# Kernel optimization log

Measured on AMD Instinct MI355X. Metric: run time of the kernel, lower is better.

Reference implementation:

```python
import jax, jax.numpy as jnp
import numpy as np

B = 16; DEMO = 5; COND = 50; QOI = 50
L = DEMO * (COND + 2 * QOI)  # 750
D = 1024; H = 16; HD = D // H; NL = 6; DFF = 4096
IN_DIM = 5; OUT_DIM = 2; MAXPOS = max(COND, QOI)
NEG = -1e9


def _build_consts():
    # token types per demo segment: 0=cond, 1=qoi_kv, 2=qoi_k (query)
    types, demo, pos = [], [], []
    for d in range(DEMO):
        types += [0] * COND + [1] * QOI + [2] * QOI
        demo += [d] * (COND + 2 * QOI)
        pos += list(range(COND)) + list(range(QOI)) + list(range(QOI))
    t = np.array(types); g = np.array(demo); p = np.array(pos)
    ti, tj = t[:, None], t[None, :]
    gi, gj = g[:, None], g[None, :]
    eye = np.arange(L)[:, None] == np.arange(L)[None, :]
    prev = (gj < gi) & (tj < 2)                      # attend to cond/qoi_kv of earlier demos
    same = (gj == gi) & ((tj == 0) | ((ti == 1) & (tj == 1)) | ((ti == 2) & eye))
    mask = prev | same                               # True = allowed
    out_idx = np.where(t == 2)[0]                    # qoi_k positions -> outputs
    return mask, p, out_idx


def setup_inputs():
    key = jax.random.key(0)
    ks = jax.random.split(key, 10)
    mask, pos, out_idx = _build_consts()
    s = 0.02
    return {
        'sequence': jax.random.normal(ks[0], (B, L, IN_DIM), jnp.float32),
        'pre_W': jax.random.normal(ks[1], (IN_DIM, D), jnp.float32) * s,
        'pre_b': jnp.zeros((D,), jnp.float32),
        'pe_table': jax.random.normal(ks[2], (MAXPOS, D), jnp.float32) * s,
        'Wqkv': jax.random.normal(ks[3], (NL, D, 3 * D), jnp.float32) * s,
        'bqkv': jnp.zeros((NL, 3 * D), jnp.float32),
        'Wo': jax.random.normal(ks[4], (NL, D, D), jnp.float32) * s,
        'bo': jnp.zeros((NL, D), jnp.float32),
        'ln1_g': jnp.ones((NL, D), jnp.float32), 'ln1_b': jnp.zeros((NL, D), jnp.float32),
        'ln2_g': jnp.ones((NL, D), jnp.float32), 'ln2_b': jnp.zeros((NL, D), jnp.float32),
        'W1': jax.random.normal(ks[5], (NL, D, DFF), jnp.float32) * s,
        'b1': jnp.zeros((NL, DFF), jnp.float32),
        'W2': jax.random.normal(ks[6], (NL, DFF, D), jnp.float32) * s,
        'b2': jnp.zeros((NL, D), jnp.float32),
        'post_W': jax.random.normal(ks[7], (D, OUT_DIM), jnp.float32) * s,
        'post_b': jnp.zeros((OUT_DIM,), jnp.float32),
        'basic_mask': jnp.asarray(mask),
        'index_pos': jnp.asarray(pos, jnp.int32),
        'out_idx': jnp.asarray(out_idx, jnp.int32),
    }


def _ln(x, g, b):
    m = jnp.mean(x, axis=-1, keepdims=True)
    v = jnp.var(x, axis=-1, keepdims=True)
    return (x - m) * jax.lax.rsqrt(v + 1e-5) * g + b


def _encoder(x, bias, Wqkv, bqkv, Wo, bo, ln1_g, ln1_b, ln2_g, ln2_b, W1, b1, W2, b2):
    scale = 1.0 / np.sqrt(HD)
    for l in range(NL):
        qkv = x @ Wqkv[l] + bqkv[l]                          # [B,L,3D]
        q, k, v = jnp.split(qkv, 3, axis=-1)
        hd = lambda t: t.reshape(B, L, H, HD).transpose(0, 2, 1, 3)
        q, k, v = hd(q), hd(k), hd(v)
        sc = jnp.einsum('bhqd,bhkd->bhqk', q, k) * scale + bias
        a = jax.nn.softmax(sc, axis=-1)
        o = jnp.einsum('bhqk,bhkd->bhqd', a, v).transpose(0, 2, 1, 3).reshape(B, L, D)
        x = _ln(x + o @ Wo[l] + bo[l], ln1_g[l], ln1_b[l])   # post-LN (torch default)
        h = jax.nn.gelu(x @ W1[l] + b1[l], approximate=False)
        x = _ln(x + h @ W2[l] + b2[l], ln2_g[l], ln2_b[l])
    return x


def reference(sequence, pre_W, pre_b, pe_table, Wqkv, bqkv, Wo, bo,
              ln1_g, ln1_b, ln2_g, ln2_b, W1, b1, W2, b2,
              post_W, post_b, basic_mask, index_pos, out_idx):
    x = sequence @ pre_W + pre_b + pe_table[index_pos]       # pre-projection + learned PE
    bias = jnp.where(basic_mask, 0.0, NEG)[None, None, :, :]  # ~basic_mask -> -inf additive
    x = _encoder(x, bias, Wqkv, bqkv, Wo, bo, ln1_g, ln1_b, ln2_g, ln2_b, W1, b1, W2, b2)
    y = x @ post_W + post_b                                  # [B,L,OUT_DIM]
    y = y[:, out_idx, :]                                     # select qoi_k outputs
    return y.reshape(B, DEMO, QOI, OUT_DIM)
```

## Files before the change

kernel.cpp:

```cpp
#include <hip/hip_runtime.h>


#define Bz  16
#define Lz  750
#define Dz  1024
#define Hz  16
#define HDz 64
#define NLz 6
#define DFFz 4096
#define Mz  (Bz*Lz)
#define MTt 94
#define VSTRIDE 768
#define QKVPART ((size_t)Bz*Hz*Lz*HDz)

typedef unsigned short u16;
typedef unsigned int   u32;
typedef unsigned long long u64;
typedef __attribute__((ext_vector_type(8))) short bf8;
typedef __attribute__((ext_vector_type(8))) unsigned short u16x8;
typedef __attribute__((ext_vector_type(4))) float f4;
typedef __attribute__((ext_vector_type(4))) unsigned short u16x4;

__device__ __forceinline__ u16 f2b(float f){
  u32 u = __builtin_bit_cast(u32, f);
  u += 0x7fffu + ((u >> 16) & 1u);
  return (u16)(u >> 16);
}
__device__ __forceinline__ u32 cvtpk(float a, float b){
  u32 r;
  asm("v_cvt_pk_bf16_f32 %0, %1, %2" : "=v"(r) : "v"(a), "v"(b));
  return r;
}
__device__ __forceinline__ void glds16(const void* g, void* l){
  __builtin_amdgcn_global_load_lds((const __attribute__((address_space(1))) void*)g,
                                   (__attribute__((address_space(3))) void*)l, 16, 0, 0);
}

__global__ __launch_bounds__(256) void k_mask(u64* __restrict__ mb){
  const int idx = blockIdx.x*256 + threadIdx.x;
  if (idx >= Lz*12) return;
  const int q = idx / 12, kt = idx - q*12;
  const int gq = q/150, rq = q - gq*150;
  const int tq = rq < 50 ? 0 : (rq < 100 ? 1 : 2);
  u64 m = 0;
  for (int j = 0; j < 64; j++){
    const int k = kt*64 + j;
    if (k >= Lz) break;
    const int gk = k/150, rk = k - gk*150;
    const int tk = rk < 50 ? 0 : (rk < 100 ? 1 : 2);
    const bool prev = (gk < gq) && (tk < 2);
    const bool same = (gk == gq) && ((tk == 0) || (tq == 1 && tk == 1) || (tq == 2 && k == q));
    if (prev || same) m |= (1ull << j);
  }
  mb[idx] = m;
}

__global__ __launch_bounds__(256) void k_embed(const float* __restrict__ seq,
    const float* __restrict__ preW, const float* __restrict__ preb,
    const float* __restrict__ pe, float* __restrict__ x, u16* __restrict__ xb){
  const int m = blockIdx.x, t = threadIdx.x;
  const int l = m % Lz;
  const int r = l % 150;
  const int p = r < 50 ? r : (r < 100 ? r - 50 : r - 100);
  const float s0 = seq[m*5+0], s1 = seq[m*5+1], s2 = seq[m*5+2],
              s3 = seq[m*5+3], s4 = seq[m*5+4];
  const int d = t*4;
  f4 acc = *(const f4*)&preb[d];
  acc += *(const f4*)&pe[p*Dz + d];
  acc += s0 * *(const f4*)&preW[0*Dz + d];
  acc += s1 * *(const f4*)&preW[1*Dz + d];
  acc += s2 * *(const f4*)&preW[2*Dz + d];
  acc += s3 * *(const f4*)&preW[3*Dz + d];
  acc += s4 * *(const f4*)&preW[4*Dz + d];
  *(f4*)&x[(size_t)m*Dz + d] = acc;
  u16x4 hv = { f2b(acc.x), f2b(acc.y), f2b(acc.z), f2b(acc.w) };
  *(u16x4*)&xb[(size_t)m*Dz + d] = hv;
}

__global__ __launch_bounds__(256) void k_transpose(const float* __restrict__ W,
    u16* __restrict__ Wt, int K, int ldw){
  __shared__ float tile[64][69];
  const int t = threadIdx.x;
  const int n0 = blockIdx.x*64, k0 = blockIdx.y*64;
  const int tx = t & 15, ty = t >> 4;
  #pragma unroll
  for (int i = 0; i < 4; i++){
    const int k = ty + i*16;
    *(f4*)&tile[k][tx*4] = *(const f4*)&W[(size_t)(k0+k)*ldw + n0 + tx*4];
  }
  __syncthreads();
  const int nx = t >> 2, kq = t & 3;
  u16 buf[16];
  #pragma unroll
  for (int e = 0; e < 16; e++)
    buf[e] = f2b(tile[kq*16 + e][nx]);
  u16x8 lo = { buf[0], buf[1], buf[2], buf[3], buf[4], buf[5], buf[6], buf[7] };
  u16x8 hi = { buf[8], buf[9], buf[10], buf[11], buf[12], buf[13], buf[14], buf[15] };
  u16* dst = &Wt[(size_t)(n0 + nx)*K + k0 + kq*16];
  *(u16x8*)dst = lo;
  *(u16x8*)(dst + 8) = hi;
}

template<int EPI>
__global__ __launch_bounds__(256, 4) void k_gemm(
    const u16* __restrict__ A, const u16* __restrict__ Bt,
    int M, int N, int K, int lda, int ldc, int col0, int NTn,
    const float* __restrict__ bias,
    float* __restrict__ xres, u16* __restrict__ outb, u16* __restrict__ vtb){
  const int id = blockIdx.x;
  const int PN = NTn << 3;
  const int panel = id / PN, rem = id - panel*PN;
  const int mt = panel*8 + (rem & 7);
  if (mt >= MTt) return;
  const int m0 = mt*128, n0 = (rem >> 3)*128;
  __shared__ u16 As[128*64];
  __shared__ u16 Bs[128*64];
  const int t = threadIdx.x;
  const int w = t >> 6, lane = t & 63;
  const int wm = (w >> 1)*64, wn = (w & 1)*64;
  const int cl = lane & 15, g4 = lane >> 4;
  f4 acc[4][4] = {};
  const int srow = t >> 3, sg = t & 7;
  const int scol = (sg ^ (srow & 7)) * 8;
  const int lds_off = srow*64 + sg*8;
  for (int k0 = 0; k0 < K; k0 += 64){
    #pragma unroll
    for (int c = 0; c < 4; c++){
      int ra = m0 + c*32 + srow; ra = ra < M ? ra : M-1;
      glds16(A + (size_t)ra*lda + k0 + scol, &As[c*2048 + lds_off]);
      const int rb = n0 + c*32 + srow;
      glds16(Bt + (size_t)rb*K + k0 + scol, &Bs[c*2048 + lds_off]);
    }
    __syncthreads();
    #pragma unroll
    for (int kk = 0; kk < 2; kk++){
      const int ko = ((kk*4 + g4) ^ (cl & 7)) * 8;
      bf8 af[4], bfr[4];
      #pragma unroll
      for (int i = 0; i < 4; i++) af[i]  = *(const bf8*)&As[(wm + i*16 + cl)*64 + ko];
      #pragma unroll
      for (int j = 0; j < 4; j++) bfr[j] = *(const bf8*)&Bs[(wn + j*16 + cl)*64 + ko];
      #pragma unroll
      for (int i = 0; i < 4; i++)
        #pragma unroll
        for (int j = 0; j < 4; j++)
          acc[i][j] = __builtin_amdgcn_mfma_f32_16x16x32_bf16(af[i], bfr[j], acc[i][j], 0, 0, 0);
    }
    __syncthreads();
  }
  const int rl = g4*4;
  #pragma unroll
  for (int i = 0; i < 4; i++){
    #pragma unroll
    for (int j = 0; j < 4; j++){
      const int gn = n0 + wn + j*16 + cl;
      const float bsv = bias ? bias[gn] : 0.f;
      if constexpr (EPI == 0){
        const int part = gn >> 10;
        const int hh = (gn >> 6) & 15;
        const int dd = gn & 63;
        const int gm0 = m0 + wm + i*16 + rl;
        if (part == 2){
          if (gm0 + 3 < M){
            const int b = gm0 / Lz, lr0 = gm0 - b*Lz;
            const float v0 = acc[i][j][0] + bsv, v1 = acc[i][j][1] + bsv;
            const float v2 = acc[i][j][2] + bsv, v3 = acc[i][j][3] + bsv;
            if (lr0 <= Lz - 4){
              u32* dst = (u32*)&vtb[((size_t)(b*Hz + hh)*HDz + dd)*VSTRIDE + lr0];
              dst[0] = cvtpk(v0, v1);
              dst[1] = cvtpk(v2, v3);
            } else {
              #pragma unroll
              for (int r = 0; r < 4; r++){
                const int gm = gm0 + r;
                const int br = gm / Lz, lr = gm - br*Lz;
                vtb[((size_t)(br*Hz + hh)*HDz + dd)*VSTRIDE + lr] = f2b(acc[i][j][r] + bsv);
              }
            }
          }
        } else {
          #pragma unroll
          for (int r = 0; r < 4; r++){
            const int gm = gm0 + r;
            if (gm < M){
              const int b = gm / Lz, lr = gm - b*Lz;
              outb[(size_t)part*QKVPART + ((size_t)(b*Hz + hh)*Lz + lr)*HDz + dd]
                  = f2b(acc[i][j][r] + bsv);
            }
          }
        }
      } else {
        #pragma unroll
        for (int r = 0; r < 4; r++){
          const int gm = m0 + wm + i*16 + rl + r;
          if (gm < M){
            const float v = acc[i][j][r] + bsv;
            if constexpr (EPI == 1){
              xres[(size_t)gm*ldc + col0 + gn] += v;
            } else {
              const float ge = 0.5f*v*(1.0f + erff(v*0.70710678f));
              outb[(size_t)gm*ldc + col0 + gn] = f2b(ge);
            }
          }
        }
      }
    }
  }
}

__global__ __launch_bounds__(64, 4) void k_attn(const u16* __restrict__ qb,
    const u16* __restrict__ kb, const u16* __restrict__ vt,
    const u64* __restrict__ mb, u16* __restrict__ ob){
  __shared__ u32 Ps[1024];
  const int t = threadIdx.x;
  const int cl = t & 15, g4 = t >> 4;
  const int id = blockIdx.x;
  const int xcd = id & 7, j = id >> 3;
  const int bh = xcd*32 + (j/12);
  const int bx = j - (j/12)*12;
  const int b = bh >> 4, h = bh & 15;
  const u16* qhp = qb + (size_t)bh*(Lz*HDz);
  const u16* khp = kb + (size_t)bh*(Lz*HDz);
  const u16* vhp = vt + (size_t)bh*(HDz*VSTRIDE);
  const float SC = 0.18033688011112042f;
  const f4 z4 = {0.f, 0.f, 0.f, 0.f};

  for (int half = 0; half < 2; half++){
    const int c = half ? (23 - bx) : bx;
    const int q0 = c*32;
    bf8 qfr[2][2];
    int qc[2];
    #pragma unroll
    for (int qf = 0; qf < 2; qf++){
      const int q = q0 + qf*16 + cl;
      qc[qf] = q < Lz ? q : Lz-1;
      #pragma unroll
      for (int kk = 0; kk < 2; kk++)
        qfr[qf][kk] = *(const bf8*)&qhp[(size_t)qc[qf]*HDz + kk*32 + g4*8];
    }
    int qmax = q0 + 31; if (qmax > Lz-1) qmax = Lz-1;
    const int gqm = qmax/150;
    int kmax = gqm*150 + 100; if (qmax + 1 > kmax) kmax = qmax + 1;
    const int nt = (kmax + 63) >> 6;

    f4 oacc[4][2] = {};
    float mrun[2] = {-1e30f, -1e30f}, lrun[2] = {0.f, 0.f};

    for (int kt = 0; kt < nt; kt++){
      const int kstart = kt*64;
      u32 mlo[2], mhi[2];
      #pragma unroll
      for (int qf = 0; qf < 2; qf++){
        const u64 m = mb[qc[qf]*12 + kt];
        mlo[qf] = (u32)m; mhi[qf] = (u32)(m >> 32);
      }
      f4 sacc[4][2];
      __builtin_amdgcn_s_setprio(1);
      #pragma unroll
      for (int kk = 0; kk < 2; kk++){
        bf8 kfr[4];
        #pragma unroll
        for (int kf = 0; kf < 4; kf++)
          kfr[kf] = *(const bf8*)&khp[(size_t)(kstart + kf*16 + cl)*HDz + kk*32 + g4*8];
        #pragma unroll
        for (int kf = 0; kf < 4; kf++)
          #pragma unroll
          for (int qf = 0; qf < 2; qf++)
            sacc[kf][qf] = __builtin_amdgcn_mfma_f32_16x16x32_bf16(kfr[kf], qfr[qf][kk],
                             kk == 0 ? z4 : sacc[kf][qf], 0, 0, 0);
      }
      __builtin_amdgcn_s_setprio(0);
      float own0 = -1e30f, own1 = -1e30f;
      #pragma unroll
      for (int kf = 0; kf < 4; kf++){
        #pragma unroll
        for (int rr = 0; rr < 4; rr++){
          const float s0 = sacc[kf][0][rr]*SC;
          const float s1 = sacc[kf][1][rr]*SC;
          sacc[kf][0][rr] = s0; sacc[kf][1][rr] = s1;
          own0 = fmaxf(own0, s0); own1 = fmaxf(own1, s1);
        }
      }
      own0 = fmaxf(own0, __shfl_xor(own0, 16)); own0 = fmaxf(own0, __shfl_xor(own0, 32));
      own1 = fmaxf(own1, __shfl_xor(own1, 16)); own1 = fmaxf(own1, __shfl_xor(own1, 32));
      const float mn0 = fmaxf(mrun[0], own0), mn1 = fmaxf(mrun[1], own1);
      const float sc0 = exp2f(mrun[0] - mn0), sc1 = exp2f(mrun[1] - mn1);
      float sum0 = 0.f, sum1 = 0.f;
      #pragma unroll
      for (int kf = 0; kf < 4; kf++){
        #pragma unroll
        for (int qf = 0; qf < 2; qf++){
          const float mn = qf ? mn1 : mn0;
          const u32 w16 = ((kf & 2) ? mhi[qf] : mlo[qf]) >> ((kf & 1)*16);
          const u32 wq = w16 >> (g4*4);
          f4 p;
          #pragma unroll
          for (int rr = 0; rr < 4; rr++){
            const float pe = exp2f(sacc[kf][qf][rr] - mn);
            p[rr] = ((wq >> rr) & 1u) ? pe : 0.f;
            if (qf == 0) sum0 += p[rr]; else sum1 += p[rr];
          }
          const u32 lo = cvtpk(p[0], p[1]);
          const u32 hi = cvtpk(p[2], p[3]);
          const int kk = kf >> 1;
          const int tg4 = ((kf & 1) << 1) | (g4 >> 1);
          const int widx = (qf*2 + kk)*256 + tg4*64 + cl*4 + (g4 & 1)*2;
          *(u64*)&Ps[widx] = ((u64)hi << 32) | lo;
        }
      }
      sum0 += __shfl_xor(sum0, 16); sum0 += __shfl_xor(sum0, 32);
      sum1 += __shfl_xor(sum1, 16); sum1 += __shfl_xor(sum1, 32);
      lrun[0] = lrun[0]*sc0 + sum0; mrun[0] = mn0;
      lrun[1] = lrun[1]*sc1 + sum1; mrun[1] = mn1;
      #pragma unroll
      for (int df = 0; df < 4; df++){
        oacc[df][0] *= sc0;
        oacc[df][1] *= sc1;
      }
      __builtin_amdgcn_s_setprio(1);
      #pragma unroll
      for (int kk = 0; kk < 2; kk++){
        bf8 vfr[4];
        #pragma unroll
        for (int df = 0; df < 4; df++)
          vfr[df] = *(const bf8*)&vhp[(size_t)(df*16 + cl)*VSTRIDE + kstart + kk*32 + g4*8];
        bf8 pw[2];
        #pragma unroll
        for (int qf = 0; qf < 2; qf++)
          pw[qf] = *(const bf8*)&Ps[(qf*2 + kk)*256 + g4*64 + cl*4];
        #pragma unroll
        for (int df = 0; df < 4; df++)
          #pragma unroll
          for (int qf = 0; qf < 2; qf++)
            oacc[df][qf] = __builtin_amdgcn_mfma_f32_16x16x32_bf16(vfr[df], pw[qf], oacc[df][qf], 0, 0, 0);
      }
      __builtin_amdgcn_s_setprio(0);
    }
    #pragma unroll
    for (int qf = 0; qf < 2; qf++){
      const int q = q0 + qf*16 + cl;
      if (q < Lz){
        const float inv = 1.f / lrun[qf];
        #pragma unroll
        for (int df = 0; df < 4; df++){
          u16x4 hv = { f2b(oacc[df][qf][0]*inv), f2b(oacc[df][qf][1]*inv),
                       f2b(oacc[df][qf][2]*inv), f2b(oacc[df][qf][3]*inv) };
          *(u16x4*)&ob[((size_t)b*Lz + q)*Dz + h*HDz + df*16 + g4*4] = hv;
        }
      }
    }
  }
}

__global__ __launch_bounds__(256) void k_ln(float* __restrict__ x, u16* __restrict__ xb,
    const float* __restrict__ g, const float* __restrict__ bb){
  const int m = blockIdx.x, t = threadIdx.x;
  float* xr = x + (size_t)m*Dz;
  f4 v = *(const f4*)&xr[t*4];
  float s = v.x + v.y + v.z + v.w;
  float q = v.x*v.x + v.y*v.y + v.z*v.z + v.w*v.w;
  #pragma unroll
  for (int off = 1; off < 64; off <<= 1){
    s += __shfl_xor(s, off);
    q += __shfl_xor(q, off);
  }
  __shared__ float ss[4], sq[4];
  const int w = t >> 6;
  if ((t & 63) == 0){ ss[w] = s; sq[w] = q; }
  __syncthreads();
  s = ss[0] + ss[1] + ss[2] + ss[3];
  q = sq[0] + sq[1] + sq[2] + sq[3];
  const float mean = s * (1.f/1024.f);
  const float var  = q * (1.f/1024.f) - mean*mean;
  const float rs = rsqrtf(var + 1e-5f);
  const f4 gg = *(const f4*)&g[t*4];
  const f4 bv = *(const f4*)&bb[t*4];
  f4 o;
  o.x = (v.x - mean)*rs*gg.x + bv.x;
  o.y = (v.y - mean)*rs*gg.y + bv.y;
  o.z = (v.z - mean)*rs*gg.z + bv.z;
  o.w = (v.w - mean)*rs*gg.w + bv.w;
  *(f4*)&xr[t*4] = o;
  u16x4 hv = { f2b(o.x), f2b(o.y), f2b(o.z), f2b(o.w) };
  *(u16x4*)&xb[(size_t)m*Dz + t*4] = hv;
}

__global__ __launch_bounds__(64) void k_out(const float* __restrict__ x,
    const float* __restrict__ pw, const float* __restrict__ pb, float* __restrict__ out){
  const int bid = blockIdx.x, lane = threadIdx.x;
  const int b = bid / 250, oi = bid - b*250;
  const int dd = oi / 50, qq = oi - dd*50;
  const int l = dd*150 + 100 + qq;
  const float* xr = x + ((size_t)b*Lz + l)*Dz;
  float a0 = 0.f, a1 = 0.f;
  #pragma unroll
  for (int c = 0; c < 4; c++){
    const int d = c*256 + lane*4;
    const f4 v  = *(const f4*)&xr[d];
    const f4 p0 = *(const f4*)&pw[2*d];
    const f4 p1 = *(const f4*)&pw[2*d + 4];
    a0 += v.x*p0.x + v.y*p0.z + v.z*p1.x + v.w*p1.z;
    a1 += v.x*p0.y + v.y*p0.w + v.z*p1.y + v.w*p1.w;
  }
  #pragma unroll
  for (int off = 32; off > 0; off >>= 1){
    a0 += __shfl_xor(a0, off);
    a1 += __shfl_xor(a1, off);
  }
  if (lane == 0){
    out[(size_t)bid*2 + 0] = a0 + pb[0];
    out[(size_t)bid*2 + 1] = a1 + pb[1];
  }
}

extern "C" void kernel_launch(void* const* d_in, const int* in_sizes, int n_in,
                              void* d_out, int out_size, void* d_ws, size_t ws_size,
                              hipStream_t stream){
  (void)in_sizes; (void)n_in; (void)out_size; (void)ws_size;
  const float* seq   = (const float*)d_in[0];
  const float* preW  = (const float*)d_in[1];
  const float* preb  = (const float*)d_in[2];
  const float* pe    = (const float*)d_in[3];
  const float* Wqkv  = (const float*)d_in[4];
  const float* bqkv  = (const float*)d_in[5];
  const float* Wo    = (const float*)d_in[6];
  const float* bo    = (const float*)d_in[7];
  const float* ln1g  = (const float*)d_in[8];
  const float* ln1b  = (const float*)d_in[9];
  const float* ln2g  = (const float*)d_in[10];
  const float* ln2b  = (const float*)d_in[11];
  const float* W1    = (const float*)d_in[12];
  const float* b1    = (const float*)d_in[13];
  const float* W2    = (const float*)d_in[14];
  const float* b2    = (const float*)d_in[15];
  const float* postW = (const float*)d_in[16];
  const float* postb = (const float*)d_in[17];
  float* out = (float*)d_out;

  char* ws = (char*)d_ws;
  float* x  = (float*)(ws + 0);
  u16*   xb = (u16*)(ws + 49152000);
  u16*   R  = (u16*)(ws + 73728000);
  u16* qB = R;
  u16* kB = R + QKVPART;
  u16* oB = R + 2*QKVPART;
  u16* vT = (u16*)(ws + 147456000);
  u16* wt = (u16*)(ws + 172621824);
  u64* mbp = (u64*)(ws + 178913280);
  u16* hB = R;

  k_mask<<<36, 256, 0, stream>>>(mbp);
  k_embed<<<Mz, 256, 0, stream>>>(seq, preW, preb, pe, x, xb);
  for (int l = 0; l < NLz; l++){
    k_transpose<<<dim3(48, 16), 256, 0, stream>>>(Wqkv + (size_t)l*1024*3072, wt, 1024, 3072);
    k_gemm<0><<<12*8*24, 256, 0, stream>>>(xb, wt, Mz, 3072, 1024, 1024, 0, 0, 24,
                                           bqkv + l*3072, nullptr, qB, vT);
    k_attn<<<3072, 64, 0, stream>>>(qB, kB, vT, mbp, oB);
    k_transpose<<<dim3(16, 16), 256, 0, stream>>>(Wo + (size_t)l*1024*1024, wt, 1024, 1024);
    k_gemm<1><<<12*8*8, 256, 0, stream>>>(oB, wt, Mz, 1024, 1024, 1024, 1024, 0, 8,
                                          bo + l*1024, x, nullptr, nullptr);
    k_ln<<<Mz, 256, 0, stream>>>(x, xb, ln1g + l*1024, ln1b + l*1024);
    for (int off = 0; off < 4096; off += 2048){
      k_transpose<<<dim3(32, 16), 256, 0, stream>>>(W1 + (size_t)l*1024*4096 + off, wt, 1024, 4096);
      k_gemm<2><<<12*8*16, 256, 0, stream>>>(xb, wt, Mz, 2048, 1024, 1024, 4096, off, 16,
                                             b1 + l*4096 + off, nullptr, hB, nullptr);
    }
    for (int koff = 0; koff < 4096; koff += 2048){
      k_transpose<<<dim3(16, 32), 256, 0, stream>>>(W2 + (size_t)l*4096*1024 + (size_t)koff*1024,
                                                    wt, 2048, 1024);
      k_gemm<1><<<12*8*8, 256, 0, stream>>>(hB + koff, wt, Mz, 1024, 2048, 4096, 1024, 0, 8,
                                            koff == 0 ? (b2 + l*1024) : nullptr, x, nullptr, nullptr);
    }
    k_ln<<<Mz, 256, 0, stream>>>(x, xb, ln2g + l*1024, ln2b + l*1024);
  }
  k_out<<<4000, 64, 0, stream>>>(x, postW, postb, out);
}
```

Before: 3.913 ms.

## Double-buffer GEMM LDS tiles with async prefetch two stages ahead

```diff
diff --git a/kernel.cpp b/kernel.cpp
--- a/kernel.cpp
+++ b/kernel.cpp
@@ -102,7 +102,7 @@
 }
 
 template<int EPI>
-__global__ __launch_bounds__(256, 4) void k_gemm(
+__global__ __launch_bounds__(256, 2) void k_gemm(
     const u16* __restrict__ A, const u16* __restrict__ Bt,
     int M, int N, int K, int lda, int ldc, int col0, int NTn,
     const float* __restrict__ bias,
@@ -113,8 +113,8 @@
   const int mt = panel*8 + (rem & 7);
   if (mt >= MTt) return;
   const int m0 = mt*128, n0 = (rem >> 3)*128;
-  __shared__ u16 As[128*64];
-  __shared__ u16 Bs[128*64];
+  __shared__ u16 As[2][128*64];
+  __shared__ u16 Bs[2][128*64];
   const int t = threadIdx.x;
   const int w = t >> 6, lane = t & 63;
   const int wm = (w >> 1)*64, wn = (w & 1)*64;
@@ -123,31 +123,49 @@
   const int srow = t >> 3, sg = t & 7;
   const int scol = (sg ^ (srow & 7)) * 8;
   const int lds_off = srow*64 + sg*8;
-  for (int k0 = 0; k0 < K; k0 += 64){
-    #pragma unroll
-    for (int c = 0; c < 4; c++){
-      int ra = m0 + c*32 + srow; ra = ra < M ? ra : M-1;
-      glds16(A + (size_t)ra*lda + k0 + scol, &As[c*2048 + lds_off]);
-      const int rb = n0 + c*32 + srow;
-      glds16(Bt + (size_t)rb*K + k0 + scol, &Bs[c*2048 + lds_off]);
-    }
-    __syncthreads();
+
+#define STG(c, kt) do {                                                          \
+    _Pragma("unroll")                                                            \
+    for (int cc = 0; cc < 4; cc++){                                              \
+      int ra = m0 + cc*32 + srow; ra = ra < M ? ra : M-1;                        \
+      glds16(A + (size_t)ra*lda + (size_t)(kt)*64 + scol, &As[c][cc*2048 + lds_off]); \
+      const int rb = n0 + cc*32 + srow;                                          \
+      glds16(Bt + (size_t)rb*K + (size_t)(kt)*64 + scol, &Bs[c][cc*2048 + lds_off]); \
+    }                                                                            \
+  } while(0)
+
+  const int nt = K >> 6;
+  STG(0, 0); STG(1, 1);
+  for (int kt = 0; kt < nt; kt++){
+    const int c = kt & 1;
+    if (kt + 1 < nt) asm volatile("s_waitcnt vmcnt(8)" ::: "memory");
+    else             asm volatile("s_waitcnt vmcnt(0)" ::: "memory");
+    __builtin_amdgcn_s_barrier();
+    bf8 af[4][2], bfr[4][2];
     #pragma unroll
     for (int kk = 0; kk < 2; kk++){
       const int ko = ((kk*4 + g4) ^ (cl & 7)) * 8;
-      bf8 af[4], bfr[4];
-      #pragma unroll
-      for (int i = 0; i < 4; i++) af[i]  = *(const bf8*)&As[(wm + i*16 + cl)*64 + ko];
-      #pragma unroll
-      for (int j = 0; j < 4; j++) bfr[j] = *(const bf8*)&Bs[(wn + j*16 + cl)*64 + ko];
+      #pragma unroll
+      for (int i = 0; i < 4; i++) af[i][kk]  = *(const bf8*)&As[c][(wm + i*16 + cl)*64 + ko];
+      #pragma unroll
+      for (int j = 0; j < 4; j++) bfr[j][kk] = *(const bf8*)&Bs[c][(wn + j*16 + cl)*64 + ko];
+    }
+    asm volatile("s_waitcnt lgkmcnt(0)" ::: "memory");
+    __builtin_amdgcn_sched_barrier(0);
+    __builtin_amdgcn_s_barrier();
+    if (kt + 2 < nt) STG(c, kt + 2);
+    __builtin_amdgcn_s_setprio(1);
+    #pragma unroll
+    for (int kk = 0; kk < 2; kk++)
       #pragma unroll
       for (int i = 0; i < 4; i++)
         #pragma unroll
         for (int j = 0; j < 4; j++)
-          acc[i][j] = __builtin_amdgcn_mfma_f32_16x16x32_bf16(af[i], bfr[j], acc[i][j], 0, 0, 0);
-    }
-    __syncthreads();
-  }
+          acc[i][j] = __builtin_amdgcn_mfma_f32_16x16x32_bf16(af[i][kk], bfr[j][kk], acc[i][j], 0, 0, 0);
+    __builtin_amdgcn_s_setprio(0);
+  }
+#undef STG
+
   const int rl = g4*4;
   #pragma unroll
   for (int i = 0; i < 4; i++){
```

Measured after the change: 4.497 ms. 14.9% more time.

## Split attention key tiles across two waves with LDS softmax merge

Applied to the files above, without the earlier changes.

```diff
diff --git a/kernel.cpp b/kernel.cpp
--- a/kernel.cpp
+++ b/kernel.cpp
@@ -102,7 +102,7 @@
 }
 
 template<int EPI>
-__global__ __launch_bounds__(256, 4) void k_gemm(
+__global__ __launch_bounds__(256, 5) void k_gemm(
     const u16* __restrict__ A, const u16* __restrict__ Bt,
     int M, int N, int K, int lda, int ldc, int col0, int NTn,
     const float* __restrict__ bias,
@@ -208,12 +208,14 @@
   }
 }
 
-__global__ __launch_bounds__(64, 4) void k_attn(const u16* __restrict__ qb,
+__global__ __launch_bounds__(128, 5) void k_attn(const u16* __restrict__ qb,
     const u16* __restrict__ kb, const u16* __restrict__ vt,
     const u64* __restrict__ mb, u16* __restrict__ ob){
-  __shared__ u32 Ps[1024];
-  const int t = threadIdx.x;
-  const int cl = t & 15, g4 = t >> 4;
+  __shared__ u32 Ps[2][1024];
+  __shared__ float Om[64*32];
+  __shared__ float Ml[64*4];
+  const int t = threadIdx.x, wid = t >> 6, lane = t & 63;
+  const int cl = lane & 15, g4 = lane >> 4;
   const int id = blockIdx.x;
   const int xcd = id & 7, j = id >> 3;
   const int bh = xcd*32 + (j/12);
@@ -222,6 +224,7 @@
   const u16* qhp = qb + (size_t)bh*(Lz*HDz);
   const u16* khp = kb + (size_t)bh*(Lz*HDz);
   const u16* vhp = vt + (size_t)bh*(HDz*VSTRIDE);
+  u32* myPs = &Ps[wid][0];
   const float SC = 0.18033688011112042f;
   const f4 z4 = {0.f, 0.f, 0.f, 0.f};
 
@@ -246,7 +249,7 @@
     f4 oacc[4][2] = {};
     float mrun[2] = {-1e30f, -1e30f}, lrun[2] = {0.f, 0.f};
 
-    for (int kt = 0; kt < nt; kt++){
+    for (int kt = wid; kt < nt; kt += 2){
       const int kstart = kt*64;
       u32 mlo[2], mhi[2];
       #pragma unroll
@@ -305,7 +308,7 @@
           const int kk = kf >> 1;
           const int tg4 = ((kf & 1) << 1) | (g4 >> 1);
           const int widx = (qf*2 + kk)*256 + tg4*64 + cl*4 + (g4 & 1)*2;
-          *(u64*)&Ps[widx] = ((u64)hi << 32) | lo;
+          *(u64*)&myPs[widx] = ((u64)hi << 32) | lo;
         }
       }
       sum0 += __shfl_xor(sum0, 16); sum0 += __shfl_xor(sum0, 32);
@@ -327,7 +330,7 @@
         bf8 pw[2];
         #pragma unroll
         for (int qf = 0; qf < 2; qf++)
-          pw[qf] = *(const bf8*)&Ps[(qf*2 + kk)*256 + g4*64 + cl*4];
+          pw[qf] = *(const bf8*)&myPs[(qf*2 + kk)*256 + g4*64 + cl*4];
         #pragma unroll
         for (int df = 0; df < 4; df++)
           #pragma unroll
@@ -336,19 +339,43 @@
       }
       __builtin_amdgcn_s_setprio(0);
     }
-    #pragma unroll
-    for (int qf = 0; qf < 2; qf++){
-      const int q = q0 + qf*16 + cl;
-      if (q < Lz){
-        const float inv = 1.f / lrun[qf];
-        #pragma unroll
-        for (int df = 0; df < 4; df++){
-          u16x4 hv = { f2b(oacc[df][qf][0]*inv), f2b(oacc[df][qf][1]*inv),
-                       f2b(oacc[df][qf][2]*inv), f2b(oacc[df][qf][3]*inv) };
-          *(u16x4*)&ob[((size_t)b*Lz + q)*Dz + h*HDz + df*16 + g4*4] = hv;
+    __syncthreads();
+    if (wid == 1){
+      #pragma unroll
+      for (int df = 0; df < 4; df++)
+        #pragma unroll
+        for (int qf = 0; qf < 2; qf++)
+          *(f4*)&Om[lane*32 + (df*2 + qf)*4] = oacc[df][qf];
+      Ml[lane*4 + 0] = mrun[0]; Ml[lane*4 + 1] = mrun[1];
+      Ml[lane*4 + 2] = lrun[0]; Ml[lane*4 + 3] = lrun[1];
+    }
+    __syncthreads();
+    if (wid == 0){
+      const float m1a = Ml[lane*4 + 0], m1b = Ml[lane*4 + 1];
+      const float l1a = Ml[lane*4 + 2], l1b = Ml[lane*4 + 3];
+      const float M0 = fmaxf(mrun[0], m1a), M1 = fmaxf(mrun[1], m1b);
+      const float sA0 = exp2f(mrun[0] - M0), sB0 = exp2f(m1a - M0);
+      const float sA1 = exp2f(mrun[1] - M1), sB1 = exp2f(m1b - M1);
+      const float L0 = lrun[0]*sA0 + l1a*sB0;
+      const float L1 = lrun[1]*sA1 + l1b*sB1;
+      const float inv0 = 1.f / L0, inv1 = 1.f / L1;
+      #pragma unroll
+      for (int qf = 0; qf < 2; qf++){
+        const int q = q0 + qf*16 + cl;
+        if (q < Lz){
+          const float sA = qf ? sA1 : sA0, sB = qf ? sB1 : sB0;
+          const float inv = qf ? inv1 : inv0;
+          #pragma unroll
+          for (int df = 0; df < 4; df++){
+            const f4 o1 = *(const f4*)&Om[lane*32 + (df*2 + qf)*4];
+            const f4 om = oacc[df][qf]*sA + o1*sB;
+            u16x4 hv = { f2b(om[0]*inv), f2b(om[1]*inv), f2b(om[2]*inv), f2b(om[3]*inv) };
+            *(u16x4*)&ob[((size_t)b*Lz + q)*Dz + h*HDz + df*16 + g4*4] = hv;
+          }
         }
       }
     }
+    __syncthreads();
   }
 }
 
@@ -455,7 +482,7 @@
     k_transpose<<<dim3(48, 16), 256, 0, stream>>>(Wqkv + (size_t)l*1024*3072, wt, 1024, 3072);
     k_gemm<0><<<12*8*24, 256, 0, stream>>>(xb, wt, Mz, 3072, 1024, 1024, 0, 0, 24,
                                            bqkv + l*3072, nullptr, qB, vT);
-    k_attn<<<3072, 64, 0, stream>>>(qB, kB, vT, mbp, oB);
+    k_attn<<<3072, 128, 0, stream>>>(qB, kB, vT, mbp, oB);
     k_transpose<<<dim3(16, 16), 256, 0, stream>>>(Wo + (size_t)l*1024*1024, wt, 1024, 1024);
     k_gemm<1><<<12*8*8, 256, 0, stream>>>(oB, wt, Mz, 1024, 1024, 1024, 1024, 0, 8,
                                           bo + l*1024, x, nullptr, nullptr);
```

New measurement: 6.704 ms. 71.3% more time.
